# Kernel optimization log

Measured on AMD Instinct MI355X. Metric: run time of the kernel, lower is better.

Reference implementation:

```python
import jax, jax.numpy as jnp
import numpy as np

N, D, C = 16384, 256, 10000
S, M = 30.0, 0.4


def setup_inputs() -> dict:
    key = jax.random.key(0)
    kx, kl, kw = jax.random.split(key, 3)
    x = jax.random.normal(kx, (N, D), dtype=jnp.float32)
    labels = jax.random.randint(kl, (N,), 0, C, dtype=jnp.int64)
    # Linear weight [out_features, in_features]; NOTE: the torch code's
    # F.normalize inside the parameter loop is a no-op (rebinds local var),
    # so W is used UN-normalized. We replicate that faithfully.
    W = jax.random.normal(kw, (C, D), dtype=jnp.float32) * (1.0 / np.sqrt(D))
    return {"x": x, "labels": labels, "W": W}


def reference(x, labels, W):
    # L2-normalize embeddings only (weight normalization in source is a no-op)
    xn = x / jnp.linalg.norm(x, axis=1, keepdims=True)  # [N, D]
    wf = xn @ W.T                                       # [N, C] cosine-ish logits
    tgt = jnp.take_along_axis(wf, labels[:, None], axis=1)[:, 0]  # wf[i, y_i]
    numerator = S * (tgt - M)
    # sum over all classes except the label (exclusion via subtraction)
    excl_sum = jnp.sum(jnp.exp(S * wf), axis=1) - jnp.exp(S * tgt)
    denominator = jnp.exp(numerator) + excl_sum
    L = numerator - jnp.log(denominator)
    return -jnp.mean(L)
```

## Files before the change

kernel.cpp:

```cpp
#include <hip/hip_runtime.h>
#include <hip/hip_bf16.h>
#include <math.h>

constexpr int N = 16384, D = 256, C = 10000;
constexpr float S = 30.0f, MARGIN = 0.4f;
constexpr int BM = 128, BN = 80;
constexpr int NX = N / BM;
constexpr int NY = C / BN;
constexpr int NWG = NX * NY;
constexpr float S_LOG2E = 43.2808512266689f;

constexpr int PREPX_BLOCKS = N / 16;
constexpr int PREPW_BLOCKS = C / 16;

using bf16 = __hip_bfloat16;
typedef __attribute__((ext_vector_type(4))) int   int4v;
typedef __attribute__((ext_vector_type(8))) int   int8v;
typedef __attribute__((ext_vector_type(4))) float f32x4;

#define DRAIN_DMA()                                        \
    do {                                                   \
        asm volatile("s_waitcnt vmcnt(0)" ::: "memory");   \
        __builtin_amdgcn_sched_barrier(0);                 \
    } while (0)

__device__ inline int pk4_fp8(float e0, float e1, float e2, float e3) {
    int lo = __builtin_amdgcn_cvt_pk_fp8_f32(e0, e1, 0, false);
    return  __builtin_amdgcn_cvt_pk_fp8_f32(e2, e3, lo, true);
}

__global__ __launch_bounds__(256) void prep(const float* __restrict__ x,
                                            const int* __restrict__ labels,
                                            const float* __restrict__ W,
                                            char* __restrict__ Af,
                                            float* __restrict__ tgt,
                                            char* __restrict__ Bf,
                                            float* __restrict__ out) {
    const int bid = blockIdx.x;
    if (bid == 0 && threadIdx.x == 0) out[0] = 0.0f;

    const int tl = threadIdx.x;
    const int r = tl >> 4, c = tl & 15;
    auto frag_off = [&](int g16) -> size_t {
        return ((size_t)g16 * 2 + (c >> 3)) * 2048 + (size_t)(c & 1) * 1024
             + (size_t)((((c >> 1) & 3) * 16 + r)) * 16;
    };

    if (bid < PREPX_BLOCKS) {
        const int rg = bid;
        const int row = rg * 16 + r;
        const float* xr = x + (size_t)row * D + c * 16;
        f32x4 v0 = *(const f32x4*)(xr + 0);
        f32x4 v1 = *(const f32x4*)(xr + 4);
        f32x4 v2 = *(const f32x4*)(xr + 8);
        f32x4 v3 = *(const f32x4*)(xr + 12);

        float ssq = v0.x*v0.x + v0.y*v0.y + v0.z*v0.z + v0.w*v0.w
                  + v1.x*v1.x + v1.y*v1.y + v1.z*v1.z + v1.w*v1.w
                  + v2.x*v2.x + v2.y*v2.y + v2.z*v2.z + v2.w*v2.w
                  + v3.x*v3.x + v3.y*v3.y + v3.z*v3.z + v3.w*v3.w;
        ssq += __shfl_xor(ssq, 1);
        ssq += __shfl_xor(ssq, 2);
        ssq += __shfl_xor(ssq, 4);
        ssq += __shfl_xor(ssq, 8);
        float rinv = rsqrtf(ssq);

        const int lab = labels[row];
        const float* wr = W + (size_t)lab * D + c * 16;
        f32x4 w0 = *(const f32x4*)(wr + 0);
        f32x4 w1 = *(const f32x4*)(wr + 4);
        f32x4 w2 = *(const f32x4*)(wr + 8);
        f32x4 w3 = *(const f32x4*)(wr + 12);
        float td = v0.x*w0.x + v0.y*w0.y + v0.z*w0.z + v0.w*w0.w
                 + v1.x*w1.x + v1.y*w1.y + v1.z*w1.z + v1.w*w1.w
                 + v2.x*w2.x + v2.y*w2.y + v2.z*w2.z + v2.w*w2.w
                 + v3.x*w3.x + v3.y*w3.y + v3.z*w3.z + v3.w*w3.w;
        td += __shfl_xor(td, 1);
        td += __shfl_xor(td, 2);
        td += __shfl_xor(td, 4);
        td += __shfl_xor(td, 8);
        if (c == 0) tgt[row] = td * rinv;

        int4v pk;
        pk.x = pk4_fp8(v0.x * rinv, v0.y * rinv, v0.z * rinv, v0.w * rinv);
        pk.y = pk4_fp8(v1.x * rinv, v1.y * rinv, v1.z * rinv, v1.w * rinv);
        pk.z = pk4_fp8(v2.x * rinv, v2.y * rinv, v2.z * rinv, v2.w * rinv);
        pk.w = pk4_fp8(v3.x * rinv, v3.y * rinv, v3.z * rinv, v3.w * rinv);
        *(int4v*)(Af + frag_off(rg)) = pk;
    } else {
        const int rg = bid - PREPX_BLOCKS;
        const int row = rg * 16 + r;
        const float* wr = W + (size_t)row * D + c * 16;
        f32x4 v0 = *(const f32x4*)(wr + 0);
        f32x4 v1 = *(const f32x4*)(wr + 4);
        f32x4 v2 = *(const f32x4*)(wr + 8);
        f32x4 v3 = *(const f32x4*)(wr + 12);
        int4v pk;
        pk.x = pk4_fp8(v0.x, v0.y, v0.z, v0.w);
        pk.y = pk4_fp8(v1.x, v1.y, v1.z, v1.w);
        pk.z = pk4_fp8(v2.x, v2.y, v2.z, v2.w);
        pk.w = pk4_fp8(v3.x, v3.y, v3.z, v3.w);
        *(int4v*)(Bf + frag_off(rg)) = pk;
    }
}

__global__ __launch_bounds__(256) void gemm_exp(const char* __restrict__ Af,
                                                const char* __restrict__ Bf,
                                                bf16* __restrict__ partial) {
    __shared__ __align__(16) char Bs[BN * D];

    const int bid = blockIdx.x;
    const int xcd = bid & 7;
    const int idx = bid >> 3;
    const int xl  = idx & 15;
    const int y   = idx >> 4;
    const int tile_r = (xcd * 16 + xl) * BM;
    const int tile_c = y * BN;

    const int t = threadIdx.x;
    const int lane = t & 63, w = t >> 6;

    #pragma unroll
    for (int q = 0; q < 5; ++q) {
        int cch = w * 5 + q;
        const char* gb = Bf + (size_t)y * 10 * 2048 + (size_t)cch * 1024 + lane * 16;
        __builtin_amdgcn_global_load_lds(
            (const __attribute__((address_space(1))) void*)gb,
            (__attribute__((address_space(3))) void*)(Bs + cch * 1024),
            16, 0, 0);
    }

    int8v a[2][2];
    #pragma unroll
    for (int kk = 0; kk < 2; ++kk)
        #pragma unroll
        for (int m = 0; m < 2; ++m) {
            const char* base = Af + ((size_t)((tile_r >> 4) + w * 2 + m) * 2 + kk) * 2048;
            int4v lo = *(const int4v*)(base + lane * 16);
            int4v hi = *(const int4v*)(base + 1024 + lane * 16);
            a[kk][m] = int8v{lo.x, lo.y, lo.z, lo.w, hi.x, hi.y, hi.z, hi.w};
        }

    f32x4 acc[2][5] = {};

    DRAIN_DMA();
    __syncthreads();

    #pragma unroll
    for (int kk = 0; kk < 2; ++kk) {
        int8v b[5];
        #pragma unroll
        for (int n = 0; n < 5; ++n) {
            const char* base = Bs + (n * 2 + kk) * 2048;
            int4v lo = *(const int4v*)(base + lane * 16);
            int4v hi = *(const int4v*)(base + 1024 + lane * 16);
            b[n] = int8v{lo.x, lo.y, lo.z, lo.w, hi.x, hi.y, hi.z, hi.w};
        }
        #pragma unroll
        for (int m = 0; m < 2; ++m)
            #pragma unroll
            for (int n = 0; n < 5; ++n)
                acc[m][n] = __builtin_amdgcn_mfma_scale_f32_16x16x128_f8f6f4(
                    a[kk][m], b[n], acc[m][n],
                    0 , 0 ,
                    0, 0x7F7F7F7F,
                    0, 0x7F7F7F7F);
    }

    __syncthreads();
    float* eps = (float*)Bs;

    #pragma unroll
    for (int m = 0; m < 2; ++m) {
        float rs[4] = {0.f, 0.f, 0.f, 0.f};
        #pragma unroll
        for (int n = 0; n < 5; ++n) {
            #pragma unroll
            for (int r = 0; r < 4; ++r)
                rs[r] += __builtin_amdgcn_exp2f(acc[m][n][r] * S_LOG2E);
        }
        #pragma unroll
        for (int r = 0; r < 4; ++r) {
            float v = rs[r];
            v += __shfl_xor(v, 1);
            v += __shfl_xor(v, 2);
            v += __shfl_xor(v, 4);
            v += __shfl_xor(v, 8);
            if ((lane & 15) == 0)
                eps[w * 32 + m * 16 + (lane >> 4) * 4 + r] = v;
        }
    }
    __syncthreads();
    if (t < BM)
        partial[(size_t)y * N + tile_r + t] = __float2bfloat16(eps[t]);
}

__global__ __launch_bounds__(256) void loss_part(const float* __restrict__ tgt,
                                                 const bf16* __restrict__ partial,
                                                 float* __restrict__ out) {
    int i = blockIdx.x * 256 + threadIdx.x;
    float s0 = 0.f, s1 = 0.f, s2 = 0.f, s3 = 0.f, s4 = 0.f;
    #pragma unroll 1
    for (int y = 0; y < NY; y += 5) {
        s0 += __bfloat162float(partial[(size_t)(y + 0) * N + i]);
        s1 += __bfloat162float(partial[(size_t)(y + 1) * N + i]);
        s2 += __bfloat162float(partial[(size_t)(y + 2) * N + i]);
        s3 += __bfloat162float(partial[(size_t)(y + 3) * N + i]);
        s4 += __bfloat162float(partial[(size_t)(y + 4) * N + i]);
    }
    float sum = ((s0 + s1) + (s2 + s3)) + s4;

    float tg = tgt[i];
    float num = S * (tg - MARGIN);
    float den = __expf(num) + sum - __expf(S * tg);
    float L = num - logf(den);

    float v = L;
    #pragma unroll
    for (int off = 1; off < 64; off <<= 1) v += __shfl_xor(v, off);
    __shared__ float s4m[4];
    int lane = threadIdx.x & 63, w = threadIdx.x >> 6;
    if (lane == 0) s4m[w] = v;
    __syncthreads();
    if (threadIdx.x == 0) {
        float bsum = s4m[0] + s4m[1] + s4m[2] + s4m[3];
        atomicAdd(out, -bsum / (float)N);
    }
}

extern "C" void kernel_launch(void* const* d_in, const int* in_sizes, int n_in,
                              void* d_out, int out_size, void* d_ws, size_t ws_size,
                              hipStream_t stream) {
    const float* x = (const float*)d_in[0];
    const int* labels = (const int*)d_in[1];
    const float* W = (const float*)d_in[2];

    char* ws = (char*)d_ws;
    char* Af       = ws;
    char* Bf       = ws + 4194304;
    float* tgt     = (float*)(ws + 6754304);
    bf16* partial  = (bf16*)(ws + 6819840);
    float* out = (float*)d_out;

    prep<<<PREPX_BLOCKS + PREPW_BLOCKS, 256, 0, stream>>>(x, labels, W, Af, tgt, Bf, out);
    gemm_exp<<<NWG, 256, 0, stream>>>(Af, Bf, partial);
    loss_part<<<N / 256, 256, 0, stream>>>(tgt, partial, out);
}
```

Measured before the change: 92.19 us.

## Loop each workgroup over five column tiles with double-buffered B staging

Each GEMM workgroup now handles five consecutive column tiles instead of one. It keeps its fp8 A fragments in registers across those tiles and prefetches the next B tile into a second LDS buffer while computing the current one. This cuts the number of workgroups and the repeated A loads and launch overhead. The S·log2e scale is also folded into the normalized x before fp8 quantization, which removes a multiply per logit before exp2. Two risks come with this: the pre-scaled values sit in a different fp8 range, which may change accuracy, and reusing the shared eps buffer across iterations without a trailing barrier opens a possible read/write race.

```diff
diff --git a/kernel.cpp b/kernel.cpp
--- a/kernel.cpp
+++ b/kernel.cpp
@@ -5,9 +5,11 @@
 constexpr int N = 16384, D = 256, C = 10000;
 constexpr float S = 30.0f, MARGIN = 0.4f;
 constexpr int BM = 128, BN = 80;
+constexpr int YG = 5;
 constexpr int NX = N / BM;
 constexpr int NY = C / BN;
-constexpr int NWG = NX * NY;
+constexpr int NYG = NY / YG;
+constexpr int NWG = NX * NYG;
 constexpr float S_LOG2E = 43.2808512266689f;
 
 constexpr int PREPX_BLOCKS = N / 16;
@@ -81,11 +83,12 @@
         td += __shfl_xor(td, 8);
         if (c == 0) tgt[row] = td * rinv;
 
+        const float sc = rinv * S_LOG2E;
         int4v pk;
-        pk.x = pk4_fp8(v0.x * rinv, v0.y * rinv, v0.z * rinv, v0.w * rinv);
-        pk.y = pk4_fp8(v1.x * rinv, v1.y * rinv, v1.z * rinv, v1.w * rinv);
-        pk.z = pk4_fp8(v2.x * rinv, v2.y * rinv, v2.z * rinv, v2.w * rinv);
-        pk.w = pk4_fp8(v3.x * rinv, v3.y * rinv, v3.z * rinv, v3.w * rinv);
+        pk.x = pk4_fp8(v0.x * sc, v0.y * sc, v0.z * sc, v0.w * sc);
+        pk.y = pk4_fp8(v1.x * sc, v1.y * sc, v1.z * sc, v1.w * sc);
+        pk.z = pk4_fp8(v2.x * sc, v2.y * sc, v2.z * sc, v2.w * sc);
+        pk.w = pk4_fp8(v3.x * sc, v3.y * sc, v3.z * sc, v3.w * sc);
         *(int4v*)(Af + frag_off(rg)) = pk;
     } else {
         const int rg = bid - PREPX_BLOCKS;
@@ -107,29 +110,33 @@
 __global__ __launch_bounds__(256) void gemm_exp(const char* __restrict__ Af,
                                                 const char* __restrict__ Bf,
                                                 bf16* __restrict__ partial) {
-    __shared__ __align__(16) char Bs[BN * D];
+    __shared__ __align__(16) char Bs[2][BN * D];
+    __shared__ float eps[BM];
 
     const int bid = blockIdx.x;
     const int xcd = bid & 7;
     const int idx = bid >> 3;
     const int xl  = idx & 15;
-    const int y   = idx >> 4;
+    const int yg  = idx >> 4;
     const int tile_r = (xcd * 16 + xl) * BM;
-    const int tile_c = y * BN;
+    const int y0 = yg * YG;
 
     const int t = threadIdx.x;
     const int lane = t & 63, w = t >> 6;
 
-    #pragma unroll
-    for (int q = 0; q < 5; ++q) {
-        int cch = w * 5 + q;
-        const char* gb = Bf + (size_t)y * 10 * 2048 + (size_t)cch * 1024 + lane * 16;
-        __builtin_amdgcn_global_load_lds(
-            (const __attribute__((address_space(1))) void*)gb,
-            (__attribute__((address_space(3))) void*)(Bs + cch * 1024),
-            16, 0, 0);
-    }
-
+    auto STAGE = [&](int p, int b) {
+        #pragma unroll
+        for (int q = 0; q < 5; ++q) {
+            int cch = w * 5 + q;
+            const char* gb = Bf + (size_t)(y0 + p) * 10 * 2048 + (size_t)cch * 1024 + lane * 16;
+            __builtin_amdgcn_global_load_lds(
+                (const __attribute__((address_space(1))) void*)gb,
+                (__attribute__((address_space(3))) void*)(&Bs[b][0] + cch * 1024),
+                16, 0, 0);
+        }
+    };
+
+    STAGE(0, 0);
     int8v a[2][2];
     #pragma unroll
     for (int kk = 0; kk < 2; ++kk)
@@ -140,59 +147,61 @@
             int4v hi = *(const int4v*)(base + 1024 + lane * 16);
             a[kk][m] = int8v{lo.x, lo.y, lo.z, lo.w, hi.x, hi.y, hi.z, hi.w};
         }
-
-    f32x4 acc[2][5] = {};
-
     DRAIN_DMA();
     __syncthreads();
 
     #pragma unroll
-    for (int kk = 0; kk < 2; ++kk) {
-        int8v b[5];
-        #pragma unroll
-        for (int n = 0; n < 5; ++n) {
-            const char* base = Bs + (n * 2 + kk) * 2048;
-            int4v lo = *(const int4v*)(base + lane * 16);
-            int4v hi = *(const int4v*)(base + 1024 + lane * 16);
-            b[n] = int8v{lo.x, lo.y, lo.z, lo.w, hi.x, hi.y, hi.z, hi.w};
-        }
-        #pragma unroll
-        for (int m = 0; m < 2; ++m)
-            #pragma unroll
-            for (int n = 0; n < 5; ++n)
-                acc[m][n] = __builtin_amdgcn_mfma_scale_f32_16x16x128_f8f6f4(
-                    a[kk][m], b[n], acc[m][n],
-                    0 , 0 ,
-                    0, 0x7F7F7F7F,
-                    0, 0x7F7F7F7F);
-    }
-
-    __syncthreads();
-    float* eps = (float*)Bs;
-
-    #pragma unroll
-    for (int m = 0; m < 2; ++m) {
-        float rs[4] = {0.f, 0.f, 0.f, 0.f};
-        #pragma unroll
-        for (int n = 0; n < 5; ++n) {
-            #pragma unroll
-            for (int r = 0; r < 4; ++r)
-                rs[r] += __builtin_amdgcn_exp2f(acc[m][n][r] * S_LOG2E);
-        }
-        #pragma unroll
-        for (int r = 0; r < 4; ++r) {
-            float v = rs[r];
-            v += __shfl_xor(v, 1);
-            v += __shfl_xor(v, 2);
-            v += __shfl_xor(v, 4);
-            v += __shfl_xor(v, 8);
-            if ((lane & 15) == 0)
-                eps[w * 32 + m * 16 + (lane >> 4) * 4 + r] = v;
-        }
-    }
-    __syncthreads();
-    if (t < BM)
-        partial[(size_t)y * N + tile_r + t] = __float2bfloat16(eps[t]);
+    for (int p = 0; p < YG; ++p) {
+        const int cur = p & 1;
+        if (p + 1 < YG) STAGE(p + 1, cur ^ 1);
+
+        f32x4 acc[2][5] = {};
+        #pragma unroll
+        for (int kk = 0; kk < 2; ++kk) {
+            int8v b[5];
+            #pragma unroll
+            for (int n = 0; n < 5; ++n) {
+                const char* base = &Bs[cur][0] + (n * 2 + kk) * 2048;
+                int4v lo = *(const int4v*)(base + lane * 16);
+                int4v hi = *(const int4v*)(base + 1024 + lane * 16);
+                b[n] = int8v{lo.x, lo.y, lo.z, lo.w, hi.x, hi.y, hi.z, hi.w};
+            }
+            #pragma unroll
+            for (int m = 0; m < 2; ++m)
+                #pragma unroll
+                for (int n = 0; n < 5; ++n)
+                    acc[m][n] = __builtin_amdgcn_mfma_scale_f32_16x16x128_f8f6f4(
+                        a[kk][m], b[n], acc[m][n],
+                        0 , 0 ,
+                        0, 0x7F7F7F7F,
+                        0, 0x7F7F7F7F);
+        }
+
+        #pragma unroll
+        for (int m = 0; m < 2; ++m) {
+            float rs[4] = {0.f, 0.f, 0.f, 0.f};
+            #pragma unroll
+            for (int n = 0; n < 5; ++n) {
+                #pragma unroll
+                for (int r = 0; r < 4; ++r)
+                    rs[r] += __builtin_amdgcn_exp2f(acc[m][n][r]);
+            }
+            #pragma unroll
+            for (int r = 0; r < 4; ++r) {
+                float v = rs[r];
+                v += __shfl_xor(v, 1);
+                v += __shfl_xor(v, 2);
+                v += __shfl_xor(v, 4);
+                v += __shfl_xor(v, 8);
+                if ((lane & 15) == 0)
+                    eps[w * 32 + m * 16 + (lane >> 4) * 4 + r] = v;
+            }
+        }
+        DRAIN_DMA();
+        __syncthreads();
+        if (t < BM)
+            partial[(size_t)(y0 + p) * N + tile_r + t] = __float2bfloat16(eps[t]);
+    }
 }
 
 __global__ __launch_bounds__(256) void loss_part(const float* __restrict__ tgt,
```

Result: slower. 112.1 us (+21.7%).
